# Kernel optimization log

Measured on AMD Instinct MI355X. Metric: run time of the kernel, lower is better.

## Reference

```python
import jax, jax.numpy as jnp
import numpy as np

D_MODEL = 1024
NUM_HEADS = 16
DEPTH = D_MODEL // NUM_HEADS


def setup_inputs() -> dict:
    key = jax.random.key(0)
    ks = jax.random.split(key, 9)
    B, S = 2, 2048
    scale = 1.0 / np.sqrt(D_MODEL)
    x = jax.random.normal(ks[0], (B, S, D_MODEL), dtype=jnp.float32)
    wq = jax.random.normal(ks[1], (D_MODEL, D_MODEL), dtype=jnp.float32) * scale
    wk = jax.random.normal(ks[2], (D_MODEL, D_MODEL), dtype=jnp.float32) * scale
    wv = jax.random.normal(ks[3], (D_MODEL, D_MODEL), dtype=jnp.float32) * scale
    wo = jax.random.normal(ks[4], (D_MODEL, D_MODEL), dtype=jnp.float32) * scale
    bq = jnp.zeros((D_MODEL,), dtype=jnp.float32)
    bk = jnp.zeros((D_MODEL,), dtype=jnp.float32)
    bv = jnp.zeros((D_MODEL,), dtype=jnp.float32)
    bo = jnp.zeros((D_MODEL,), dtype=jnp.float32)
    return {"x": x, "wq": wq, "bq": bq, "wk": wk, "bk": bk,
            "wv": wv, "bv": bv, "wo": wo, "bo": bo}


def _split_heads(t):
    # [B, S, D] -> [B, H, S, depth]
    B, S, _ = t.shape
    return t.reshape(B, S, NUM_HEADS, DEPTH).transpose(0, 2, 1, 3)


def reference(x, wq, bq, wk, bk, wv, bv, wo, bo):
    q = _split_heads(x @ wq + bq)
    k = _split_heads(x @ wk + bk)
    v = _split_heads(x @ wv + bv)
    # scaled dot-product attention with materialized [B,H,S,S] scores
    logits = jnp.einsum("bhqd,bhkd->bhqk", q, k) / jnp.sqrt(
        jnp.asarray(DEPTH, dtype=x.dtype))
    attn = jax.nn.softmax(logits, axis=-1)
    out = jnp.einsum("bhqk,bhkd->bhqd", attn, v)
    B, _, S, _ = out.shape
    concat = out.transpose(0, 2, 1, 3).reshape(B, S, D_MODEL)
    return concat @ wo + bo
```

## Files before the change

kernel.cpp:

```cpp
#include <hip/hip_runtime.h>
#include <hip/hip_bf16.h>
#include <stdint.h>

typedef unsigned short u16;
typedef __attribute__((ext_vector_type(8))) short short8;
typedef __attribute__((ext_vector_type(4))) float f32x4;

__device__ __forceinline__ float bf2f(u16 u) {
    union { uint32_t u; float f; } v; v.u = ((uint32_t)u) << 16; return v.f;
}
__device__ __forceinline__ u16 f2bf(float f) {
    union { float f; uint32_t u; } v; v.f = f;
    uint32_t r = (v.u + 0x7fffu + ((v.u >> 16) & 1u)) >> 16;
    return (u16)r;
}
__device__ __forceinline__ uint32_t pkbf(float a, float b) {
    union { __hip_bfloat162 h; uint32_t w; } u;
    u.h = __float22bfloat162_rn(float2{a, b});
    return u.w;
}
__device__ __forceinline__ void store_out(u16* p, float v) { *p = f2bf(v); }
__device__ __forceinline__ void store_out(float* p, float v) { *p = v; }

__device__ __forceinline__ void async_ld16(const u16* g, u16* l) {
    __builtin_amdgcn_global_load_lds(
        (const __attribute__((address_space(1))) void*)g,
        (__attribute__((address_space(3))) void*)l, 16, 0, 0);
}

__global__ void prep(const float* __restrict__ x,
                     const float* __restrict__ w0, const float* __restrict__ w1,
                     const float* __restrict__ w2, const float* __restrict__ w3,
                     u16* __restrict__ xb, u16* __restrict__ wT,
                     u16* __restrict__ woT) {
    const int z = blockIdx.z;
    __shared__ u16 tile[64][65];
    const int tid = threadIdx.x;
    if (z == 3 || z == 4) {
        const int blk = (z - 3) * 256 + blockIdx.y * 16 + blockIdx.x;
#pragma unroll
        for (int it = 0; it < 4; it++) {
            size_t i = (size_t)blk * 8192 + (size_t)it * 2048 + (size_t)tid * 8;
            float4 a = *(const float4*)(x + i);
            float4 b = *(const float4*)(x + i + 4);
            union { uint32_t w[4]; uint4 v; } o;
            o.w[0] = pkbf(a.x, a.y); o.w[1] = pkbf(a.z, a.w);
            o.w[2] = pkbf(b.x, b.y); o.w[3] = pkbf(b.z, b.w);
            *(uint4*)(xb + i) = o.v;
        }
        return;
    }
    const float* in = (z == 0) ? w0 : (z == 1) ? w1 : (z == 2) ? w2 : w3;
    u16* o = (z < 3) ? (wT + (size_t)z * 1024 * 1024) : woT;
    const int xr = tid & 31, yr = tid >> 5;
    const int gx = blockIdx.x * 64, gy = blockIdx.y * 64;
#pragma unroll
    for (int jj = 0; jj < 8; jj++) {
        int row = yr + jj * 8;
        float2 v = *(const float2*)(in + (size_t)(gy + row) * 1024 + gx + 2 * xr);
        tile[row][2 * xr] = f2bf(v.x);
        tile[row][2 * xr + 1] = f2bf(v.y);
    }
    __syncthreads();
#pragma unroll
    for (int ww = 0; ww < 4; ww++) {
        int s = tid + ww * 256;
        int r = s >> 4, c0 = (s & 15) * 4;
        union { u16 u[4]; uint2 v; } p;
#pragma unroll
        for (int i = 0; i < 4; i++) p.u[i] = tile[c0 + i][r];
        *(uint2*)(o + (size_t)(gx + r) * 1024 + gy + c0) = p.v;
    }
}

__global__ void transpose1(const float* __restrict__ w, u16* __restrict__ out) {
    __shared__ u16 tile[32][33];
    int x = blockIdx.x * 32 + threadIdx.x;
    int y0 = blockIdx.y * 32;
#pragma unroll
    for (int j = threadIdx.y; j < 32; j += 8)
        tile[j][threadIdx.x] = f2bf(w[(size_t)(y0 + j) * 1024 + x]);
    __syncthreads();
    int ox = blockIdx.y * 32 + threadIdx.x;
    int oy0 = blockIdx.x * 32;
#pragma unroll
    for (int j = threadIdx.y; j < 32; j += 8)
        out[(size_t)(oy0 + j) * 1024 + ox] = tile[threadIdx.x][j];
}

#define GBM 128
#define GBN 128
#define GBK 32

template <typename OutT>
__global__ __launch_bounds__(256) void gemm_bt(
    const u16* __restrict__ A, int lda,
    const u16* __restrict__ BT, int ldb,
    const float* __restrict__ bias0, const float* __restrict__ bias1,
    const float* __restrict__ bias2,
    OutT* __restrict__ C, int ldc, int K) {
    __shared__ __align__(16) u16 As[2][GBM * GBK];
    __shared__ __align__(16) u16 Bs[2][GBN * GBK];

    const int tid = threadIdx.x;
    const int wave = tid >> 6, lane = tid & 63;
    const int quad = lane >> 4, l16 = lane & 15;
    const int wr = wave >> 1, wc = wave & 1;

    int bx = blockIdx.x, by = blockIdx.y;
    if (gridDim.x == 24 && gridDim.y == 32) {
        const int wgid = blockIdx.x + blockIdx.y * 24;
        const int xcd = wgid & 7, t = wgid >> 3;
        bx = (xcd & 1) * 12 + t % 12;
        by = (xcd >> 1) * 8 + t / 12;
    }
    const int m0 = by * GBM, n0 = bx * GBN;

    const int seg = n0 >> 10;
    const float* bsel = (seg == 0) ? bias0 : (seg == 1) ? bias1 : bias2;

    f32x4 acc[4][4] = {};

    const int srow = tid >> 2;
    const int scol = (tid & 3) * 8;
    const u16* Ag0 = A + (size_t)(m0 + srow) * lda + scol;
    const u16* Ag1 = Ag0 + (size_t)64 * lda;
    const u16* Bg0 = BT + (size_t)(n0 + srow) * ldb + scol;
    const u16* Bg1 = Bg0 + (size_t)64 * ldb;
    const int woff = wave << 9;

    async_ld16(Ag0, As[0] + woff);
    async_ld16(Ag1, As[0] + woff + 64 * GBK);
    async_ld16(Bg0, Bs[0] + woff);
    async_ld16(Bg1, Bs[0] + woff + 64 * GBK);

    int cur = 0;
    for (int kb = 0; kb < K; kb += GBK) {
        __syncthreads();

        if (kb + GBK < K) {
            const int nxt = cur ^ 1;
            async_ld16(Ag0 + kb + GBK, As[nxt] + woff);
            async_ld16(Ag1 + kb + GBK, As[nxt] + woff + 64 * GBK);
            async_ld16(Bg0 + kb + GBK, Bs[nxt] + woff);
            async_ld16(Bg1 + kb + GBK, Bs[nxt] + woff + 64 * GBK);
        }

        short8 af[4], bf[4];
#pragma unroll
        for (int mt = 0; mt < 4; mt++)
            af[mt] = *(const short8*)(As[cur] + (wr * 64 + mt * 16 + l16) * GBK + quad * 8);
#pragma unroll
        for (int nt = 0; nt < 4; nt++)
            bf[nt] = *(const short8*)(Bs[cur] + (wc * 64 + nt * 16 + l16) * GBK + quad * 8);
#pragma unroll
        for (int mt = 0; mt < 4; mt++)
#pragma unroll
            for (int nt = 0; nt < 4; nt++)
                acc[mt][nt] = __builtin_amdgcn_mfma_f32_16x16x32_bf16(
                    af[mt], bf[nt], acc[mt][nt], 0, 0, 0);
        cur ^= 1;
    }

#pragma unroll
    for (int nt = 0; nt < 4; nt++) {
        int col = n0 + wc * 64 + nt * 16 + l16;
        float bv = bsel[col & 1023];
#pragma unroll
        for (int mt = 0; mt < 4; mt++) {
            int row = m0 + wr * 64 + mt * 16 + quad * 4;
#pragma unroll
            for (int r = 0; r < 4; r++)
                store_out(&C[(size_t)(row + r) * ldc + col], acc[mt][nt][r] + bv);
        }
    }
}

__global__ __launch_bounds__(256) void gemm_bt64(
    const u16* __restrict__ A, int lda,
    const u16* __restrict__ BT, int ldb,
    const float* __restrict__ bias,
    float* __restrict__ C, int ldc, int K) {
    __shared__ __align__(16) u16 As[2][64 * GBK];
    __shared__ __align__(16) u16 Bs[2][128 * GBK];

    const int tid = threadIdx.x;
    const int wave = tid >> 6, lane = tid & 63;
    const int quad = lane >> 4, l16 = lane & 15;

    int bx = blockIdx.x, by = blockIdx.y;
    if (gridDim.x == 8 && gridDim.y == 64) {
        const int wgid = blockIdx.x + blockIdx.y * 8;
        const int xcd = wgid & 7, t = wgid >> 3;
        bx = t & 7;
        by = (xcd << 3) + (t >> 3);
    }
    const int m0 = by * 64, n0 = bx * 128;

    f32x4 acc[4][2] = {};

    const int srow = tid >> 2;
    const int scol = (tid & 3) * 8;
    const u16* Ag0 = A + (size_t)(m0 + srow) * lda + scol;
    const u16* Bg0 = BT + (size_t)(n0 + srow) * ldb + scol;
    const u16* Bg1 = Bg0 + (size_t)64 * ldb;
    const int woff = wave << 9;

    async_ld16(Ag0, As[0] + woff);
    async_ld16(Bg0, Bs[0] + woff);
    async_ld16(Bg1, Bs[0] + woff + 64 * GBK);

    int cur = 0;
    for (int kb = 0; kb < K; kb += GBK) {
        __syncthreads();

        if (kb + GBK < K) {
            const int nxt = cur ^ 1;
            async_ld16(Ag0 + kb + GBK, As[nxt] + woff);
            async_ld16(Bg0 + kb + GBK, Bs[nxt] + woff);
            async_ld16(Bg1 + kb + GBK, Bs[nxt] + woff + 64 * GBK);
        }

        short8 af[4], bf[2];
#pragma unroll
        for (int mt = 0; mt < 4; mt++)
            af[mt] = *(const short8*)(As[cur] + (mt * 16 + l16) * GBK + quad * 8);
#pragma unroll
        for (int nt = 0; nt < 2; nt++)
            bf[nt] = *(const short8*)(Bs[cur] + (wave * 32 + nt * 16 + l16) * GBK + quad * 8);
#pragma unroll
        for (int mt = 0; mt < 4; mt++)
#pragma unroll
            for (int nt = 0; nt < 2; nt++)
                acc[mt][nt] = __builtin_amdgcn_mfma_f32_16x16x32_bf16(
                    af[mt], bf[nt], acc[mt][nt], 0, 0, 0);
        cur ^= 1;
    }

#pragma unroll
    for (int nt = 0; nt < 2; nt++) {
        int col = n0 + wave * 32 + nt * 16 + l16;
        float bv = bias[col & 1023];
#pragma unroll
        for (int mt = 0; mt < 4; mt++) {
            int row = m0 + mt * 16 + quad * 4;
#pragma unroll
            for (int r = 0; r < 4; r++)
                C[(size_t)(row + r) * ldc + col] = acc[mt][nt][r] + bv;
        }
    }
}

#define SEQ 2048
#define BQT 128
#define BKV 128
#define LDK 72
#define LDKV 136

__global__ __launch_bounds__(256) void attn(u16* __restrict__ QKV) {
    __shared__ __align__(16) u16 Ks[BKV * LDK];
    __shared__ __align__(16) u16 Vs[64 * LDKV];

    const int tid = threadIdx.x;
    const int wave = tid >> 6, lane = tid & 63;
    const int quad = lane >> 4, l16 = lane & 15;

    const int lin = blockIdx.x + blockIdx.y * 16 + blockIdx.z * 256;
    const int xcd = lin & 7, tswz = lin >> 3;
    const int h  = (xcd >> 1) | ((tswz & 3) << 2);
    const int qb = ((xcd & 1) << 3) | ((tswz >> 2) & 7);
    const int bb = tswz >> 5;
    const int q0 = qb * BQT;
    const size_t tok0 = (size_t)bb * SEQ;

    const u16* Qb = QKV + tok0 * 3072 + h * 64;
    const u16* Kb = QKV + tok0 * 3072 + 1024 + h * 64;
    const u16* Vb = QKV + tok0 * 3072 + 2048 + h * 64;

    const float cs = 0.18033688011112042f;

    int qr[2];
    qr[0] = q0 + wave * 16 + l16;
    qr[1] = qr[0] + 64;
    short8 aq[2][2];
#pragma unroll
    for (int s = 0; s < 2; s++) {
        union { short8 v; u16 u[8]; uint32_t w[4]; } qa, qb_;
        qa.v = *(const short8*)(Qb + (size_t)qr[s] * 3072 + quad * 8);
        qb_.v = *(const short8*)(Qb + (size_t)qr[s] * 3072 + 32 + quad * 8);
#pragma unroll
        for (int j = 0; j < 4; j++) {
            qa.w[j] = pkbf(bf2f(qa.u[2 * j]) * cs, bf2f(qa.u[2 * j + 1]) * cs);
            qb_.w[j] = pkbf(bf2f(qb_.u[2 * j]) * cs, bf2f(qb_.u[2 * j + 1]) * cs);
        }
        aq[s][0] = qa.v; aq[s][1] = qb_.v;
    }

    f32x4 o[2][4] = {};
    f32x4 o_l[2] = {};

    const short8 vone = {16256, 16256, 16256, 16256,
                         16256, 16256, 16256, 16256};

    const int srow = tid >> 2;
    const int scc = (tid & 3) * 16;
    const int pr = tid & 63;
    const int dg = wave;

    const u16* kg = Kb + (size_t)srow * 3072 + scc;
    const u16* vg = Vb + (size_t)(2 * pr) * 3072 + dg * 16;

    const int kvb = 2 * pr;
    const int kvp = (kvb & 96) | (((kvb >> 2) & 3) << 3) |
                    (((kvb >> 4) & 1) << 2) | (kvb & 3);

    uint4 k0r = *(const uint4*)(kg);
    uint4 k1r = *(const uint4*)(kg + 8);
    uint4 k2r = *(const uint4*)(kg + (size_t)64 * 3072);
    uint4 k3r = *(const uint4*)(kg + (size_t)64 * 3072 + 8);
    uint4 va0 = *(const uint4*)(vg);
    uint4 va1 = *(const uint4*)(vg + 8);
    uint4 vb0 = *(const uint4*)(vg + 3072);
    uint4 vb1 = *(const uint4*)(vg + 3072 + 8);

    for (int j0 = 0; j0 < SEQ; j0 += BKV) {
        *(uint4*)(Ks + srow * LDK + scc) = k0r;
        *(uint4*)(Ks + srow * LDK + scc + 8) = k1r;
        *(uint4*)(Ks + (srow + 64) * LDK + scc) = k2r;
        *(uint4*)(Ks + (srow + 64) * LDK + scc + 8) = k3r;
        {
            union { uint4 v[2]; u16 u[16]; } a, b;
            a.v[0] = va0; a.v[1] = va1; b.v[0] = vb0; b.v[1] = vb1;
#pragma unroll
            for (int j = 0; j < 16; j++) {
                uint32_t w = (uint32_t)a.u[j] | ((uint32_t)b.u[j] << 16);
                *(uint32_t*)(Vs + (dg * 16 + j) * LDKV + kvp) = w;
            }
        }
        __syncthreads();

        if (j0 + BKV < SEQ) {
            size_t off = (size_t)(j0 + BKV) * 3072;
            k0r = *(const uint4*)(kg + off);
            k1r = *(const uint4*)(kg + off + 8);
            k2r = *(const uint4*)(kg + off + (size_t)64 * 3072);
            k3r = *(const uint4*)(kg + off + (size_t)64 * 3072 + 8);
            va0 = *(const uint4*)(vg + off);
            va1 = *(const uint4*)(vg + off + 8);
            vb0 = *(const uint4*)(vg + off + 3072);
            vb1 = *(const uint4*)(vg + off + 3072 + 8);
        }

        f32x4 st[2][8];
        __builtin_amdgcn_s_setprio(1);
#pragma unroll
        for (int kkt = 0; kkt < 8; kkt++) {
            f32x4 s0 = {}, s1 = {};
#pragma unroll
            for (int k2 = 0; k2 < 2; k2++) {
                short8 ak = *(const short8*)(Ks + (kkt * 16 + l16) * LDK + k2 * 32 + quad * 8);
                s0 = __builtin_amdgcn_mfma_f32_16x16x32_bf16(ak, aq[0][k2], s0, 0, 0, 0);
                s1 = __builtin_amdgcn_mfma_f32_16x16x32_bf16(ak, aq[1][k2], s1, 0, 0, 0);
            }
            st[0][kkt] = s0; st[1][kkt] = s1;
        }
        __builtin_amdgcn_s_setprio(0);

#pragma unroll
        for (int s = 0; s < 2; s++)
#pragma unroll
            for (int kkt = 0; kkt < 8; kkt++)
#pragma unroll
                for (int r = 0; r < 4; r++)
                    st[s][kkt][r] = __builtin_amdgcn_exp2f(st[s][kkt][r]);

        __builtin_amdgcn_s_setprio(1);
#pragma unroll
        for (int tt = 0; tt < 4; tt++) {
            union { uint32_t w[4]; short8 v; } bp0, bp1;
            bp0.w[0] = pkbf(st[0][2 * tt][0], st[0][2 * tt][1]);
            bp0.w[1] = pkbf(st[0][2 * tt][2], st[0][2 * tt][3]);
            bp0.w[2] = pkbf(st[0][2 * tt + 1][0], st[0][2 * tt + 1][1]);
            bp0.w[3] = pkbf(st[0][2 * tt + 1][2], st[0][2 * tt + 1][3]);
            bp1.w[0] = pkbf(st[1][2 * tt][0], st[1][2 * tt][1]);
            bp1.w[1] = pkbf(st[1][2 * tt][2], st[1][2 * tt][3]);
            bp1.w[2] = pkbf(st[1][2 * tt + 1][0], st[1][2 * tt + 1][1]);
            bp1.w[3] = pkbf(st[1][2 * tt + 1][2], st[1][2 * tt + 1][3]);

            o_l[0] = __builtin_amdgcn_mfma_f32_16x16x32_bf16(vone, bp0.v, o_l[0], 0, 0, 0);
            o_l[1] = __builtin_amdgcn_mfma_f32_16x16x32_bf16(vone, bp1.v, o_l[1], 0, 0, 0);
#pragma unroll
            for (int dt = 0; dt < 4; dt++) {
                short8 av = *(const short8*)(Vs + (dt * 16 + l16) * LDKV +
                                             tt * 32 + quad * 8);
                o[0][dt] = __builtin_amdgcn_mfma_f32_16x16x32_bf16(av, bp0.v, o[0][dt], 0, 0, 0);
                o[1][dt] = __builtin_amdgcn_mfma_f32_16x16x32_bf16(av, bp1.v, o[1][dt], 0, 0, 0);
            }
        }
        __builtin_amdgcn_s_setprio(0);

        __syncthreads();
    }

#pragma unroll
    for (int s = 0; s < 2; s++) {
        const float inv_l = 1.0f / o_l[s][0];
        u16* orow = QKV + (tok0 + qr[s]) * 3072 + h * 64;
#pragma unroll
        for (int dt = 0; dt < 4; dt++) {
            uint32_t w0 = pkbf(o[s][dt][0] * inv_l, o[s][dt][1] * inv_l);
            uint32_t w1 = pkbf(o[s][dt][2] * inv_l, o[s][dt][3] * inv_l);
            uint2 w = {w0, w1};
            *(uint2*)(orow + dt * 16 + quad * 4) = w;
        }
    }
}

extern "C" void kernel_launch(void* const* d_in, const int* in_sizes, int n_in,
                              void* d_out, int out_size, void* d_ws, size_t ws_size,
                              hipStream_t stream) {
    const float* x  = (const float*)d_in[0];
    const float* wq = (const float*)d_in[1];
    const float* bq = (const float*)d_in[2];
    const float* wk = (const float*)d_in[3];
    const float* bk = (const float*)d_in[4];
    const float* wv = (const float*)d_in[5];
    const float* bv = (const float*)d_in[6];
    const float* wo = (const float*)d_in[7];
    const float* bo = (const float*)d_in[8];
    (void)in_sizes; (void)n_in; (void)out_size;

    u16* QKV = (u16*)d_ws;
    u16* wT  = QKV + (size_t)4096 * 3072;
    u16* xb  = wT + (size_t)3 * 1024 * 1024;
    u16* woT = xb;
    u16* woT2 = xb + (size_t)4096 * 1024;

    const size_t need = ((size_t)4096 * 3072 + (size_t)4 * 1024 * 1024 +
                         (size_t)4096 * 1024) * sizeof(u16);
    const bool fused = (ws_size >= need);

    if (fused) {
        prep<<<dim3(16, 16, 6), 256, 0, stream>>>(x, wq, wk, wv, wo,
                                                  xb, wT, woT2);
        gemm_bt<u16><<<dim3(24, 32), 256, 0, stream>>>(xb, 1024, wT, 1024,
                                                       bq, bk, bv, QKV, 3072, 1024);
        attn<<<dim3(16, 16, 2), 256, 0, stream>>>(QKV);
        gemm_bt64<<<dim3(8, 64), 256, 0, stream>>>(QKV, 3072, woT2, 1024, bo,
                                                   (float*)d_out, 1024, 1024);
    } else {
        prep<<<dim3(16, 16, 5), 256, 0, stream>>>(x, wq, wk, wv, wo,
                                                  xb, wT, woT2);
        gemm_bt<u16><<<dim3(24, 32), 256, 0, stream>>>(xb, 1024, wT, 1024,
                                                       bq, bk, bv, QKV, 3072, 1024);
        transpose1<<<dim3(32, 32), dim3(32, 8), 0, stream>>>(wo, woT);
        attn<<<dim3(16, 16, 2), 256, 0, stream>>>(QKV);
        gemm_bt64<<<dim3(8, 64), 256, 0, stream>>>(QKV, 3072, woT, 1024, bo,
                                                   (float*)d_out, 1024, 1024);
    }
}
```

Before: 191.7 us.

## Split attention over two KV halves and merge partials in a combine kernel

```diff
diff --git a/kernel.cpp b/kernel.cpp
--- a/kernel.cpp
+++ b/kernel.cpp
@@ -257,7 +257,10 @@
 #define LDK 72
 #define LDKV 136
 
-__global__ __launch_bounds__(256) void attn(u16* __restrict__ QKV) {
+template <int SPLIT>
+__global__ __launch_bounds__(256) void attn(u16* __restrict__ QKV,
+                                            float* __restrict__ oP,
+                                            float* __restrict__ lP) {
     __shared__ __align__(16) u16 Ks[BKV * LDK];
     __shared__ __align__(16) u16 Vs[64 * LDKV];
 
@@ -265,7 +268,11 @@
     const int wave = tid >> 6, lane = tid & 63;
     const int quad = lane >> 4, l16 = lane & 15;
 
-    const int lin = blockIdx.x + blockIdx.y * 16 + blockIdx.z * 256;
+    const int zz = blockIdx.z;
+    const int half = SPLIT ? (zz >> 1) : 0;
+    const int bbz = SPLIT ? (zz & 1) : zz;
+
+    const int lin = blockIdx.x + blockIdx.y * 16 + bbz * 256;
     const int xcd = lin & 7, tswz = lin >> 3;
     const int h  = (xcd >> 1) | ((tswz & 3) << 2);
     const int qb = ((xcd & 1) << 3) | ((tswz >> 2) & 7);
@@ -273,6 +280,9 @@
     const int q0 = qb * BQT;
     const size_t tok0 = (size_t)bb * SEQ;
 
+    const int jbeg = SPLIT ? half * 1024 : 0;
+    const int jend = SPLIT ? jbeg + 1024 : SEQ;
+
     const u16* Qb = QKV + tok0 * 3072 + h * 64;
     const u16* Kb = QKV + tok0 * 3072 + 1024 + h * 64;
     const u16* Vb = QKV + tok0 * 3072 + 2048 + h * 64;
@@ -314,16 +324,17 @@
     const int kvp = (kvb & 96) | (((kvb >> 2) & 3) << 3) |
                     (((kvb >> 4) & 1) << 2) | (kvb & 3);
 
-    uint4 k0r = *(const uint4*)(kg);
-    uint4 k1r = *(const uint4*)(kg + 8);
-    uint4 k2r = *(const uint4*)(kg + (size_t)64 * 3072);
-    uint4 k3r = *(const uint4*)(kg + (size_t)64 * 3072 + 8);
-    uint4 va0 = *(const uint4*)(vg);
-    uint4 va1 = *(const uint4*)(vg + 8);
-    uint4 vb0 = *(const uint4*)(vg + 3072);
-    uint4 vb1 = *(const uint4*)(vg + 3072 + 8);
-
-    for (int j0 = 0; j0 < SEQ; j0 += BKV) {
+    const size_t poff = (size_t)jbeg * 3072;
+    uint4 k0r = *(const uint4*)(kg + poff);
+    uint4 k1r = *(const uint4*)(kg + poff + 8);
+    uint4 k2r = *(const uint4*)(kg + poff + (size_t)64 * 3072);
+    uint4 k3r = *(const uint4*)(kg + poff + (size_t)64 * 3072 + 8);
+    uint4 va0 = *(const uint4*)(vg + poff);
+    uint4 va1 = *(const uint4*)(vg + poff + 8);
+    uint4 vb0 = *(const uint4*)(vg + poff + 3072);
+    uint4 vb1 = *(const uint4*)(vg + poff + 3072 + 8);
+
+    for (int j0 = jbeg; j0 < jend; j0 += BKV) {
         *(uint4*)(Ks + srow * LDK + scc) = k0r;
         *(uint4*)(Ks + srow * LDK + scc + 8) = k1r;
         *(uint4*)(Ks + (srow + 64) * LDK + scc) = k2r;
@@ -339,7 +350,7 @@
         }
         __syncthreads();
 
-        if (j0 + BKV < SEQ) {
+        if (j0 + BKV < jend) {
             size_t off = (size_t)(j0 + BKV) * 3072;
             k0r = *(const uint4*)(kg + off);
             k1r = *(const uint4*)(kg + off + 8);
@@ -402,18 +413,47 @@
         __syncthreads();
     }
 
-#pragma unroll
-    for (int s = 0; s < 2; s++) {
-        const float inv_l = 1.0f / o_l[s][0];
-        u16* orow = QKV + (tok0 + qr[s]) * 3072 + h * 64;
-#pragma unroll
-        for (int dt = 0; dt < 4; dt++) {
-            uint32_t w0 = pkbf(o[s][dt][0] * inv_l, o[s][dt][1] * inv_l);
-            uint32_t w1 = pkbf(o[s][dt][2] * inv_l, o[s][dt][3] * inv_l);
-            uint2 w = {w0, w1};
-            *(uint2*)(orow + dt * 16 + quad * 4) = w;
-        }
-    }
+    if (SPLIT) {
+#pragma unroll
+        for (int s = 0; s < 2; s++) {
+            float* orow = oP + (size_t)half * 4096 * 1024 +
+                          (size_t)(tok0 + qr[s]) * 1024 + h * 64;
+#pragma unroll
+            for (int dt = 0; dt < 4; dt++)
+                *(f32x4*)(orow + dt * 16 + quad * 4) = o[s][dt];
+            if (quad == 0)
+                lP[(size_t)half * 4096 * 16 + (tok0 + qr[s]) * 16 + h] = o_l[s][0];
+        }
+    } else {
+#pragma unroll
+        for (int s = 0; s < 2; s++) {
+            const float inv_l = 1.0f / o_l[s][0];
+            u16* orow = QKV + (tok0 + qr[s]) * 3072 + h * 64;
+#pragma unroll
+            for (int dt = 0; dt < 4; dt++) {
+                uint32_t w0 = pkbf(o[s][dt][0] * inv_l, o[s][dt][1] * inv_l);
+                uint32_t w1 = pkbf(o[s][dt][2] * inv_l, o[s][dt][3] * inv_l);
+                uint2 w = {w0, w1};
+                *(uint2*)(orow + dt * 16 + quad * 4) = w;
+            }
+        }
+    }
+}
+
+__global__ __launch_bounds__(256) void combine(const float* __restrict__ oP,
+                                               const float* __restrict__ lP,
+                                               u16* __restrict__ QKV) {
+    const size_t base = ((size_t)blockIdx.x * 256 + threadIdx.x) * 4;
+    const int tok = (int)(base >> 10);
+    const int col = (int)(base & 1023);
+    const int h = col >> 6;
+    float4 a = *(const float4*)(oP + (size_t)tok * 1024 + col);
+    float4 b = *(const float4*)(oP + (size_t)4096 * 1024 + (size_t)tok * 1024 + col);
+    const float l = lP[(size_t)tok * 16 + h] + lP[(size_t)4096 * 16 + tok * 16 + h];
+    const float inv = 1.0f / l;
+    uint2 w = {pkbf((a.x + b.x) * inv, (a.y + b.y) * inv),
+               pkbf((a.z + b.z) * inv, (a.w + b.w) * inv)};
+    *(uint2*)(QKV + (size_t)tok * 3072 + col) = w;
 }
 
 extern "C" void kernel_launch(void* const* d_in, const int* in_sizes, int n_in,
@@ -435,26 +475,35 @@
     u16* xb  = wT + (size_t)3 * 1024 * 1024;
     u16* woT = xb;
     u16* woT2 = xb + (size_t)4096 * 1024;
-
-    const size_t need = ((size_t)4096 * 3072 + (size_t)4 * 1024 * 1024 +
-                         (size_t)4096 * 1024) * sizeof(u16);
-    const bool fused = (ws_size >= need);
-
-    if (fused) {
-        prep<<<dim3(16, 16, 6), 256, 0, stream>>>(x, wq, wk, wv, wo,
-                                                  xb, wT, woT2);
+    float* oP = (float*)(woT2 + (size_t)1024 * 1024);
+    float* lP = oP + (size_t)2 * 4096 * 1024;
+
+    const size_t base_need = ((size_t)4096 * 3072 + (size_t)4 * 1024 * 1024 +
+                              (size_t)4096 * 1024) * sizeof(u16);
+    const size_t split_need = base_need +
+        ((size_t)2 * 4096 * 1024 + (size_t)2 * 4096 * 16) * sizeof(float);
+
+    if (ws_size >= split_need) {
+        prep<<<dim3(16, 16, 6), 256, 0, stream>>>(x, wq, wk, wv, wo, xb, wT, woT2);
         gemm_bt<u16><<<dim3(24, 32), 256, 0, stream>>>(xb, 1024, wT, 1024,
                                                        bq, bk, bv, QKV, 3072, 1024);
-        attn<<<dim3(16, 16, 2), 256, 0, stream>>>(QKV);
+        attn<1><<<dim3(16, 16, 4), 256, 0, stream>>>(QKV, oP, lP);
+        combine<<<4096, 256, 0, stream>>>(oP, lP, QKV);
+        gemm_bt64<<<dim3(8, 64), 256, 0, stream>>>(QKV, 3072, woT2, 1024, bo,
+                                                   (float*)d_out, 1024, 1024);
+    } else if (ws_size >= base_need) {
+        prep<<<dim3(16, 16, 6), 256, 0, stream>>>(x, wq, wk, wv, wo, xb, wT, woT2);
+        gemm_bt<u16><<<dim3(24, 32), 256, 0, stream>>>(xb, 1024, wT, 1024,
+                                                       bq, bk, bv, QKV, 3072, 1024);
+        attn<0><<<dim3(16, 16, 2), 256, 0, stream>>>(QKV, nullptr, nullptr);
         gemm_bt64<<<dim3(8, 64), 256, 0, stream>>>(QKV, 3072, woT2, 1024, bo,
                                                    (float*)d_out, 1024, 1024);
     } else {
-        prep<<<dim3(16, 16, 5), 256, 0, stream>>>(x, wq, wk, wv, wo,
-                                                  xb, wT, woT2);
+        prep<<<dim3(16, 16, 5), 256, 0, stream>>>(x, wq, wk, wv, wo, xb, wT, woT2);
         gemm_bt<u16><<<dim3(24, 32), 256, 0, stream>>>(xb, 1024, wT, 1024,
                                                        bq, bk, bv, QKV, 3072, 1024);
         transpose1<<<dim3(32, 32), dim3(32, 8), 0, stream>>>(wo, woT);
-        attn<<<dim3(16, 16, 2), 256, 0, stream>>>(QKV);
+        attn<0><<<dim3(16, 16, 2), 256, 0, stream>>>(QKV, nullptr, nullptr);
         gemm_bt64<<<dim3(8, 64), 256, 0, stream>>>(QKV, 3072, woT, 1024, bo,
                                                    (float*)d_out, 1024, 1024);
     }
```

Result: slower. 204.2 us (+6.6%).
